# Kernel tuning notes

Measured on AMD Instinct MI355X. Metric: run time of the kernel, lower is better.

## Reference

```python
import jax, jax.numpy as jnp
import numpy as np

N = 50000      # nodes
E = 800000     # edges
G = 512        # graphs
IN = 544; HID = 64; H = 4; OUT = 2
EPS = 1e-5

def setup_inputs():
    key = jax.random.key(0)
    ks = jax.random.split(key, 16)
    x = jax.random.normal(ks[0], (N, IN), jnp.float32)
    edge_index = jax.random.randint(ks[1], (2, E), 0, N, jnp.int64)
    batch = jnp.sort(jax.random.randint(ks[2], (N,), 0, G, jnp.int64))
    s = lambda k, shp, fan: jax.random.normal(k, shp, jnp.float32) / np.sqrt(fan)
    return {
        'x': x, 'edge_index': edge_index, 'batch': batch,
        'ln_g': jnp.ones((32,), jnp.float32), 'ln_b': jnp.zeros((32,), jnp.float32),
        'bn1_g': jnp.ones((512,), jnp.float32), 'bn1_b': jnp.zeros((512,), jnp.float32),
        'Wc': s(ks[3], (16, 512), 512), 'bc': jnp.zeros((16,), jnp.float32),
        'bn2_g': jnp.ones((48,), jnp.float32), 'bn2_b': jnp.zeros((48,), jnp.float32),
        'Wp': s(ks[4], (HID, 48), 48), 'bp': jnp.zeros((HID,), jnp.float32),
        'Wg': s(ks[5], (H * HID, HID), HID),
        'att_src': s(ks[6], (H, HID), HID), 'att_dst': s(ks[7], (H, HID), HID),
        'bg': jnp.zeros((H * HID,), jnp.float32),
        'bn3_g': jnp.ones((H * HID,), jnp.float32), 'bn3_b': jnp.zeros((H * HID,), jnp.float32),
        'W1': s(ks[8], (HID, H * HID), H * HID), 'b1': jnp.zeros((HID,), jnp.float32),
        'W2': s(ks[9], (OUT, HID), HID), 'b2': jnp.zeros((OUT,), jnp.float32),
    }

def _batchnorm(x, g, b):
    mu = jnp.mean(x, axis=0)
    var = jnp.var(x, axis=0)
    return (x - mu) * jax.lax.rsqrt(var + EPS) * g + b

def _forward(x, ln_g, ln_b, bn1_g, bn1_b, Wc, bc, bn2_g, bn2_b, Wp, bp,
             Wg, att_src, att_dst, bg, bn3_g, bn3_b, W1, b1, W2, b2,
             edge_index, batch):
    # feature split + norms
    x_cnn = _batchnorm(x[:, :512], bn1_g, bn1_b)
    f = x[:, 512:]
    mu = jnp.mean(f, axis=-1, keepdims=True)
    var = jnp.var(f, axis=-1, keepdims=True)
    f = (f - mu) * jax.lax.rsqrt(var + EPS) * ln_g + ln_b
    x_cnn = x_cnn @ Wc.T + bc                      # [N,16]
    z = jnp.concatenate([x_cnn, f], axis=1)        # [N,48]
    z = _batchnorm(z, bn2_g, bn2_b)
    z = jax.nn.relu(z @ Wp.T + bp)                 # [N,HID] (dropout=eval identity)
    # GATConv (concat=True, negative_slope=0.2)
    h = (z @ Wg.T).reshape(N, H, HID)              # [N,H,C]
    a_src = jnp.sum(h * att_src, axis=-1)          # [N,H]
    a_dst = jnp.sum(h * att_dst, axis=-1)          # [N,H]
    src, dst = edge_index[0], edge_index[1]
    e = jax.nn.leaky_relu(a_src[src] + a_dst[dst], 0.2)   # [E,H]
    m = jax.ops.segment_max(e, dst, num_segments=N)
    m = jnp.where(jnp.isfinite(m), m, 0.0)
    ex = jnp.exp(e - m[dst])
    s = jax.ops.segment_sum(ex, dst, num_segments=N)
    alpha = ex / jnp.maximum(s, 1e-16)[dst]               # [E,H]
    out = jax.ops.segment_sum(alpha[:, :, None] * h[src], dst, num_segments=N)
    out = out.reshape(N, H * HID) + bg
    # BatchNorm + ELU + mean pool + MLP head
    out = jax.nn.elu(_batchnorm(out, bn3_g, bn3_b))
    cnt = jax.ops.segment_sum(jnp.ones((N,), out.dtype), batch, num_segments=G)
    pooled = jax.ops.segment_sum(out, batch, num_segments=G) / jnp.maximum(cnt, 1.0)[:, None]
    hmlp = jax.nn.relu(pooled @ W1.T + b1)
    return hmlp @ W2.T + b2                        # [G,OUT]

def reference(x, edge_index, batch, ln_g, ln_b, bn1_g, bn1_b, Wc, bc, bn2_g, bn2_b,
              Wp, bp, Wg, att_src, att_dst, bg, bn3_g, bn3_b, W1, b1, W2, b2):
    return _forward(x, ln_g, ln_b, bn1_g, bn1_b, Wc, bc, bn2_g, bn2_b, Wp, bp,
                    Wg, att_src, att_dst, bg, bn3_g, bn3_b, W1, b1, W2, b2,
                    edge_index, batch)
```

## Files before the change

kernel.cpp:

```cpp
#include <hip/hip_runtime.h>

static constexpr int N_   = 50000;
static constexpr int E_   = 800000;
static constexpr int G_   = 512;
static constexpr int IN_  = 544;
static constexpr float EPS_ = 1e-5f;

static constexpr size_t OFF_BN1SUM = 0;
static constexpr size_t OFF_BN1SQ  = 2048;
static constexpr size_t OFF_BN2SUM = 4096;
static constexpr size_t OFF_BN2SQ  = 4288;
static constexpr size_t OFF_BN3SUM = 4480;
static constexpr size_t OFF_BN3SQ  = 5504;
static constexpr size_t OFF_COUNT  = 6528;
static constexpr size_t OFF_CUR    = 206528;
static constexpr size_t ZERO_BYTES = 406528;
static constexpr size_t OFF_OFFS   = 406528;
static constexpr size_t OFF_PART   = 606592;
static constexpr size_t OFF_WC2    = 606848;
static constexpr size_t OFF_C2     = 639616;
static constexpr size_t OFF_WP2    = 639744;
static constexpr size_t OFF_CP     = 652032;
static constexpr size_t OFF_WGT    = 652288;
static constexpr size_t OFF_ASRC   = 719872;
static constexpr size_t OFF_ADST   = 1519872;
static constexpr size_t OFF_SRCS   = 2319872;
static constexpr size_t OFF_Z      = 5519872;
static constexpr size_t OFF_H      = 15119872;
static constexpr size_t OFF_OUTP   = 66319872;
static constexpr size_t OFF_POOL   = 117519872;

#define DEV static __device__ __forceinline__

DEV float lrelu(float v) { return v > 0.f ? v : 0.2f * v; }
DEV unsigned short f2bf(float f) {
    unsigned u = __float_as_uint(f);
    return (unsigned short)((u + 0x7fffu + ((u >> 16) & 1u)) >> 16);
}
DEV float bf2f(unsigned short u) { return __uint_as_float(((unsigned)u) << 16); }

__global__ __launch_bounds__(512) void k_bn1_stats(
        const float* __restrict__ x, float* __restrict__ sum, float* __restrict__ sq) {
    __shared__ float4 ta[512];
    __shared__ float4 tb[512];
    int t = threadIdx.x;
    int cq = t & 127, rsub = t >> 7;
    int c4 = cq << 2;
    float4 a = make_float4(0.f, 0.f, 0.f, 0.f);
    float4 b = make_float4(0.f, 0.f, 0.f, 0.f);
    for (int r = blockIdx.x * 4 + rsub; r < N_; r += gridDim.x * 4) {
        float4 v = *(const float4*)(x + (size_t)r * IN_ + c4);
        a.x += v.x; a.y += v.y; a.z += v.z; a.w += v.w;
        b.x += v.x * v.x; b.y += v.y * v.y; b.z += v.z * v.z; b.w += v.w * v.w;
    }
    ta[t] = a; tb[t] = b;
    __syncthreads();
    if (t < 128) {
        float4 sa = ta[t], sb = tb[t];
#pragma unroll
        for (int r = 1; r < 4; r++) {
            float4 xa = ta[r * 128 + t], xb = tb[r * 128 + t];
            sa.x += xa.x; sa.y += xa.y; sa.z += xa.z; sa.w += xa.w;
            sb.x += xb.x; sb.y += xb.y; sb.z += xb.z; sb.w += xb.w;
        }
        int c = t << 2;
        atomicAdd(&sum[c + 0], sa.x); atomicAdd(&sum[c + 1], sa.y);
        atomicAdd(&sum[c + 2], sa.z); atomicAdd(&sum[c + 3], sa.w);
        atomicAdd(&sq[c + 0], sb.x);  atomicAdd(&sq[c + 1], sb.y);
        atomicAdd(&sq[c + 2], sb.z);  atomicAdd(&sq[c + 3], sb.w);
    }
}

__global__ void k_fold1(const float* __restrict__ sum, const float* __restrict__ sq,
                        const float* __restrict__ g, const float* __restrict__ b,
                        const float* __restrict__ Wc, const float* __restrict__ bc,
                        float* __restrict__ Wc2, float* __restrict__ c2) {
    __shared__ float t1[512];
    int j = threadIdx.x;
    float mu  = sum[j] / (float)N_;
    float var = sq[j] / (float)N_ - mu * mu;
    float s   = g[j] * rsqrtf(var + EPS_);
    t1[j] = b[j] - mu * s;
    for (int i = 0; i < 16; i++) Wc2[j * 16 + i] = Wc[i * 512 + j] * s;
    __syncthreads();
    if (j < 16) {
        float acc = bc[j];
        for (int k = 0; k < 512; k++) acc += t1[k] * Wc[j * 512 + k];
        c2[j] = acc;
    }
}

__global__ __launch_bounds__(512) void k_z(
        const float* __restrict__ x, const float* __restrict__ Wc2g,
        const float* __restrict__ c2g, const float* __restrict__ lng,
        const float* __restrict__ lnb, float* __restrict__ z,
        float* __restrict__ bn2sum, float* __restrict__ bn2sq) {
    __shared__ float wc2[512 * 16];
    __shared__ float c2s[16];
    __shared__ float bsum[48];
    __shared__ float bsq[48];
    int t = threadIdx.x;
    for (int q = t; q < 8192; q += 512) wc2[q] = Wc2g[q];
    if (t < 16) c2s[t] = c2g[t];
    if (t < 48) { bsum[t] = 0.f; bsq[t] = 0.f; }
    __syncthreads();
    int nd = t >> 3, i = t & 7;
    int node = blockIdx.x * 64 + nd;
    bool valid = node < N_;
    int rn = valid ? node : N_ - 1;
    const float4* xr = (const float4*)(x + (size_t)rn * IN_);
    float acc0 = c2s[i], acc1 = c2s[i + 8];
    for (int u = 0; u < 128; u++) {
        float4 xv = xr[u];
        int j4 = u * 4;
        acc0 += xv.x * wc2[(j4 + 0) * 16 + i];
        acc0 += xv.y * wc2[(j4 + 1) * 16 + i];
        acc0 += xv.z * wc2[(j4 + 2) * 16 + i];
        acc0 += xv.w * wc2[(j4 + 3) * 16 + i];
        acc1 += xv.x * wc2[(j4 + 0) * 16 + i + 8];
        acc1 += xv.y * wc2[(j4 + 1) * 16 + i + 8];
        acc1 += xv.z * wc2[(j4 + 2) * 16 + i + 8];
        acc1 += xv.w * wc2[(j4 + 3) * 16 + i + 8];
    }
    float v[4]; float sm = 0.f, sqv = 0.f;
#pragma unroll
    for (int jj = 0; jj < 4; jj++) {
        v[jj] = x[(size_t)rn * IN_ + 512 + i + 8 * jj];
        sm += v[jj]; sqv += v[jj] * v[jj];
    }
    for (int m = 1; m < 8; m <<= 1) {
        sm  += __shfl_xor(sm, m);
        sqv += __shfl_xor(sqv, m);
    }
    float mu  = sm * (1.f / 32.f);
    float var = sqv * (1.f / 32.f) - mu * mu;
    float rs  = rsqrtf(var + EPS_);
    float outc[6];
    outc[0] = acc0; outc[1] = acc1;
#pragma unroll
    for (int jj = 0; jj < 4; jj++) {
        int c = i + 8 * jj;
        outc[2 + jj] = (v[jj] - mu) * rs * lng[c] + lnb[c];
    }
    if (valid) {
        z[node * 48 + i]     = acc0;
        z[node * 48 + i + 8] = acc1;
#pragma unroll
        for (int jj = 0; jj < 4; jj++) z[node * 48 + 16 + i + 8 * jj] = outc[2 + jj];
    }
    float s6[6], q6[6];
#pragma unroll
    for (int k = 0; k < 6; k++) {
        float vv = valid ? outc[k] : 0.f;
        s6[k] = vv; q6[k] = vv * vv;
    }
#pragma unroll
    for (int m = 8; m < 64; m <<= 1) {
#pragma unroll
        for (int k = 0; k < 6; k++) {
            s6[k] += __shfl_xor(s6[k], m);
            q6[k] += __shfl_xor(q6[k], m);
        }
    }
    if ((t & 63) < 8) {
        int cols[6] = { i, i + 8, 16 + i, 24 + i, 32 + i, 40 + i };
#pragma unroll
        for (int k = 0; k < 6; k++) {
            atomicAdd(&bsum[cols[k]], s6[k]);
            atomicAdd(&bsq[cols[k]],  q6[k]);
        }
    }
    __syncthreads();
    if (t < 48) {
        atomicAdd(&bn2sum[t], bsum[t]);
        atomicAdd(&bn2sq[t],  bsq[t]);
    }
}

__global__ void k_fold2(const float* __restrict__ sum, const float* __restrict__ sq,
                        const float* __restrict__ g, const float* __restrict__ b,
                        const float* __restrict__ Wp, const float* __restrict__ bp,
                        float* __restrict__ Wp2, float* __restrict__ cp) {
    __shared__ float t2[48];
    int i = threadIdx.x;
    if (i < 48) {
        float mu  = sum[i] / (float)N_;
        float var = sq[i] / (float)N_ - mu * mu;
        float s   = g[i] * rsqrtf(var + EPS_);
        t2[i] = b[i] - mu * s;
        for (int k = 0; k < 64; k++) Wp2[i * 64 + k] = Wp[k * 48 + i] * s;
    }
    __syncthreads();
    float acc = bp[i];
    for (int j = 0; j < 48; j++) acc += t2[j] * Wp[i * 48 + j];
    cp[i] = acc;
}

__global__ void k_wgt(const float* __restrict__ Wg, float* __restrict__ Wgt) {
    int idx = blockIdx.x * 256 + threadIdx.x;
    if (idx < 16384) {
        int c = idx >> 6, k = idx & 63;
        Wgt[k * 256 + c] = Wg[idx];
    }
}

__global__ __launch_bounds__(512) void k_h2(
        const float* __restrict__ z, const float* __restrict__ Wp2g,
        const float* __restrict__ cpg, const float* __restrict__ Wgtg,
        const float* __restrict__ att_s, const float* __restrict__ att_d,
        ushort4* __restrict__ hbf, float* __restrict__ asrc, float* __restrict__ adst) {
    __shared__ float4 wgh[32 * 64];
    __shared__ float  z1t[128 * 64];
    __shared__ float  wp2[48 * 64];
    __shared__ float  cps[64];
    __shared__ float4 ats[64];
    __shared__ float4 atd[64];
    int t = threadIdx.x;
    int base = blockIdx.x * 128;
    {
        const float4* z4 = (const float4*)(z + (size_t)base * 48);
        float4* zt4 = (float4*)wgh;
        for (int q = t; q < 1536; q += 512) zt4[q] = z4[q];
    }
    for (int q = t; q < 3072; q += 512) wp2[q] = Wp2g[q];
    if (t < 64) {
        cps[t] = cpg[t];
        ats[t] = ((const float4*)att_s)[t];
        atd[t] = ((const float4*)att_d)[t];
    }
    __syncthreads();
    int w = t >> 6, l = t & 63;
    {
        float wpr[48];
#pragma unroll
        for (int j = 0; j < 48; j++) wpr[j] = wp2[j * 64 + l];
        const float* zt = (const float*)wgh;
        for (int p = 0; p < 16; p++) {
            int nd = p * 8 + w;
            float acc = cps[l];
            const float* zr = zt + nd * 48;
#pragma unroll
            for (int j = 0; j < 48; j++) acc += zr[j] * wpr[j];
            z1t[nd * 64 + l] = fmaxf(acc, 0.f);
        }
    }
    const float4* wg4 = (const float4*)Wgtg;
    float4 acc[16];
#pragma unroll
    for (int nd = 0; nd < 16; nd++) acc[nd] = make_float4(0.f, 0.f, 0.f, 0.f);
    for (int half = 0; half < 2; half++) {
        __syncthreads();
        for (int q = t; q < 2048; q += 512) wgh[q] = wg4[half * 2048 + q];
        __syncthreads();
        int kbase = half * 32;
        for (int kk = 0; kk < 32; kk++) {
            float4 wv = wgh[kk * 64 + l];
            int k = kbase + kk;
#pragma unroll
            for (int nd = 0; nd < 16; nd++) {
                float zv = z1t[(w * 16 + nd) * 64 + k];
                acc[nd].x += zv * wv.x; acc[nd].y += zv * wv.y;
                acc[nd].z += zv * wv.z; acc[nd].w += zv * wv.w;
            }
        }
    }
    float4 as4 = ats[l], ad4 = atd[l];
#pragma unroll
    for (int nd = 0; nd < 16; nd++) {
        int node = base + w * 16 + nd;
        if (node < N_) {
            ushort4 hv;
            hv.x = f2bf(acc[nd].x); hv.y = f2bf(acc[nd].y);
            hv.z = f2bf(acc[nd].z); hv.w = f2bf(acc[nd].w);
            hbf[(size_t)node * 64 + l] = hv;
            float pa = acc[nd].x * as4.x + acc[nd].y * as4.y +
                       acc[nd].z * as4.z + acc[nd].w * as4.w;
            float pb = acc[nd].x * ad4.x + acc[nd].y * ad4.y +
                       acc[nd].z * ad4.z + acc[nd].w * ad4.w;
            for (int m = 1; m < 16; m <<= 1) {
                pa += __shfl_xor(pa, m);
                pb += __shfl_xor(pb, m);
            }
            if ((l & 15) == 0) {
                asrc[node * 4 + (l >> 4)] = pa;
                adst[node * 4 + (l >> 4)] = pb;
            }
        }
    }
}

__global__ void k_hist(const int* __restrict__ ei, int* __restrict__ count) {
    int k = blockIdx.x * 256 + threadIdx.x;
    atomicAdd(&count[ei[E_ + k]], 1);
}

__global__ void k_scan1(const int* __restrict__ count, int* __restrict__ offs,
                        int* __restrict__ part) {
    __shared__ int sd[1024];
    int t = threadIdx.x;
    int idx = blockIdx.x * 1024 + t;
    int v = (idx < N_) ? count[idx] : 0;
    sd[t] = v;
    for (int off = 1; off < 1024; off <<= 1) {
        __syncthreads();
        int tmp = (t >= off) ? sd[t - off] : 0;
        __syncthreads();
        sd[t] += tmp;
    }
    if (idx < N_) offs[idx] = sd[t] - v;
    if (t == 1023) part[blockIdx.x] = sd[1023];
}
__global__ void k_scan2(int* __restrict__ part, int nb) {
    if (threadIdx.x == 0) {
        int run = 0;
        for (int i = 0; i < nb; i++) { int tv = part[i]; part[i] = run; run += tv; }
    }
}
__global__ void k_scan3(int* __restrict__ offs, const int* __restrict__ part) {
    int idx = blockIdx.x * 1024 + threadIdx.x;
    if (idx < N_) offs[idx] += part[blockIdx.x];
}

__global__ void k_scatter(const int* __restrict__ ei, const int* __restrict__ offs,
                          int* __restrict__ cur, int* __restrict__ srcsort) {
    int k = blockIdx.x * 256 + threadIdx.x;
    int src = ei[k], dst = ei[E_ + k];
    int pos = offs[dst] + atomicAdd(&cur[dst], 1);
    srcsort[pos] = src;
}

__global__ __launch_bounds__(256) void k_agg(
        const int* __restrict__ count, const int* __restrict__ offs,
        const int* __restrict__ srcsort, const float* __restrict__ asrc,
        const float* __restrict__ adst, const ushort4* __restrict__ hbf,
        const float* __restrict__ bg, float* __restrict__ outpre) {
    int w = threadIdx.x >> 6, l = threadIdx.x & 63;
    int dst = blockIdx.x * 4 + w;
    const float4* asrc4 = (const float4*)asrc;
    float4* out4 = (float4*)outpre;
    float4 bgv = ((const float4*)bg)[l];
    int deg = count[dst];
    if (deg == 0) { out4[dst * 64 + l] = bgv; return; }
    int base = offs[dst];
    float4 ad = ((const float4*)adst)[dst];
    const float NEGINF = -__builtin_inff();
    int my_src = 0;
    float4 my_e = make_float4(NEGINF, NEGINF, NEGINF, NEGINF);
    if (l < deg) {
        my_src = srcsort[base + l];
        float4 a = asrc4[my_src];
        my_e = make_float4(lrelu(a.x + ad.x), lrelu(a.y + ad.y),
                           lrelu(a.z + ad.z), lrelu(a.w + ad.w));
    }
    float4 mx = my_e;
    for (int j = l + 64; j < deg; j += 64) {
        int s2 = srcsort[base + j];
        float4 a = asrc4[s2];
        mx.x = fmaxf(mx.x, lrelu(a.x + ad.x)); mx.y = fmaxf(mx.y, lrelu(a.y + ad.y));
        mx.z = fmaxf(mx.z, lrelu(a.z + ad.z)); mx.w = fmaxf(mx.w, lrelu(a.w + ad.w));
    }
    for (int m = 1; m < 64; m <<= 1) {
        mx.x = fmaxf(mx.x, __shfl_xor(mx.x, m));
        mx.y = fmaxf(mx.y, __shfl_xor(mx.y, m));
        mx.z = fmaxf(mx.z, __shfl_xor(mx.z, m));
        mx.w = fmaxf(mx.w, __shfl_xor(mx.w, m));
    }
    float4 sv = make_float4(0.f, 0.f, 0.f, 0.f);
    if (l < deg) {
        sv.x = __expf(my_e.x - mx.x); sv.y = __expf(my_e.y - mx.y);
        sv.z = __expf(my_e.z - mx.z); sv.w = __expf(my_e.w - mx.w);
    }
    for (int j = l + 64; j < deg; j += 64) {
        int s2 = srcsort[base + j];
        float4 a = asrc4[s2];
        sv.x += __expf(lrelu(a.x + ad.x) - mx.x);
        sv.y += __expf(lrelu(a.y + ad.y) - mx.y);
        sv.z += __expf(lrelu(a.z + ad.z) - mx.z);
        sv.w += __expf(lrelu(a.w + ad.w) - mx.w);
    }
    for (int m = 1; m < 64; m <<= 1) {
        sv.x += __shfl_xor(sv.x, m); sv.y += __shfl_xor(sv.y, m);
        sv.z += __shfl_xor(sv.z, m); sv.w += __shfl_xor(sv.w, m);
    }
    int hd = l >> 4;
    float mh  = hd == 0 ? mx.x : hd == 1 ? mx.y : hd == 2 ? mx.z : mx.w;
    float sh  = hd == 0 ? sv.x : hd == 1 ? sv.y : hd == 2 ? sv.z : sv.w;
    float adh = hd == 0 ? ad.x : hd == 1 ? ad.y : hd == 2 ? ad.z : ad.w;
    float inv = 1.f / fmaxf(sh, 1e-16f);
    float4 acc = make_float4(0.f, 0.f, 0.f, 0.f);
    for (int j = 0; j < deg; j++) {
        int src; float eh;
        if (j < 64) {
            src = __shfl(my_src, j);
            float ex_ = __shfl(my_e.x, j), ey_ = __shfl(my_e.y, j);
            float ez_ = __shfl(my_e.z, j), ew_ = __shfl(my_e.w, j);
            eh = hd == 0 ? ex_ : hd == 1 ? ey_ : hd == 2 ? ez_ : ew_;
        } else {
            src = srcsort[base + j];
            float4 a = asrc4[src];
            float ah = hd == 0 ? a.x : hd == 1 ? a.y : hd == 2 ? a.z : a.w;
            eh = lrelu(ah + adh);
        }
        float wgt = __expf(eh - mh) * inv;
        ushort4 hv = hbf[(size_t)src * 64 + l];
        acc.x += wgt * bf2f(hv.x); acc.y += wgt * bf2f(hv.y);
        acc.z += wgt * bf2f(hv.z); acc.w += wgt * bf2f(hv.w);
    }
    out4[dst * 64 + l] = make_float4(acc.x + bgv.x, acc.y + bgv.y,
                                     acc.z + bgv.z, acc.w + bgv.w);
}

__global__ __launch_bounds__(256) void k_bn3_stats(
        const float* __restrict__ op, float* __restrict__ sum, float* __restrict__ sq) {
    __shared__ float4 ta[256];
    __shared__ float4 tb[256];
    int t = threadIdx.x;
    int cq = t & 63, rsub = t >> 6;
    int c4 = cq << 2;
    float4 a = make_float4(0.f, 0.f, 0.f, 0.f);
    float4 b = make_float4(0.f, 0.f, 0.f, 0.f);
    for (int r = blockIdx.x * 4 + rsub; r < N_; r += gridDim.x * 4) {
        float4 v = *(const float4*)(op + (size_t)r * 256 + c4);
        a.x += v.x; a.y += v.y; a.z += v.z; a.w += v.w;
        b.x += v.x * v.x; b.y += v.y * v.y; b.z += v.z * v.z; b.w += v.w * v.w;
    }
    ta[t] = a; tb[t] = b;
    __syncthreads();
    if (t < 64) {
        float4 sa = ta[t], sb = tb[t];
#pragma unroll
        for (int r = 1; r < 4; r++) {
            float4 xa = ta[r * 64 + t], xb = tb[r * 64 + t];
            sa.x += xa.x; sa.y += xa.y; sa.z += xa.z; sa.w += xa.w;
            sb.x += xb.x; sb.y += xb.y; sb.z += xb.z; sb.w += xb.w;
        }
        int c = t << 2;
        atomicAdd(&sum[c + 0], sa.x); atomicAdd(&sum[c + 1], sa.y);
        atomicAdd(&sum[c + 2], sa.z); atomicAdd(&sum[c + 3], sa.w);
        atomicAdd(&sq[c + 0], sb.x);  atomicAdd(&sq[c + 1], sb.y);
        atomicAdd(&sq[c + 2], sb.z);  atomicAdd(&sq[c + 3], sb.w);
    }
}

__global__ __launch_bounds__(256) void k_pool(
        const float* __restrict__ op, const int* __restrict__ batch,
        const float* __restrict__ bn3sum, const float* __restrict__ bn3sq,
        const float* __restrict__ bn3g, const float* __restrict__ bn3b,
        float* __restrict__ pooled) {
    __shared__ float4 tile[256];
    int g = blockIdx.x;
    int t = threadIdx.x;
    int cq = t & 63, rsub = t >> 6;
    int c4 = cq << 2;
    int lo = 0, hi = N_;
    while (lo < hi) { int mid = (lo + hi) >> 1; if (batch[mid] < g) lo = mid + 1; else hi = mid; }
    int start = lo;
    hi = N_;
    while (lo < hi) { int mid = (lo + hi) >> 1; if (batch[mid] < g + 1) lo = mid + 1; else hi = mid; }
    int end = lo;
    float scv[4], shv[4];
#pragma unroll
    for (int k = 0; k < 4; k++) {
        int c = c4 + k;
        float mu  = bn3sum[c] / (float)N_;
        float var = bn3sq[c] / (float)N_ - mu * mu;
        float s   = bn3g[c] * rsqrtf(var + EPS_);
        scv[k] = s; shv[k] = bn3b[c] - mu * s;
    }
    float4 acc = make_float4(0.f, 0.f, 0.f, 0.f);
    for (int n = start + rsub; n < end; n += 4) {
        float4 v = *(const float4*)(op + (size_t)n * 256 + c4);
        float e0 = v.x * scv[0] + shv[0], e1 = v.y * scv[1] + shv[1];
        float e2 = v.z * scv[2] + shv[2], e3 = v.w * scv[3] + shv[3];
        acc.x += (e0 > 0.f) ? e0 : expm1f(e0);
        acc.y += (e1 > 0.f) ? e1 : expm1f(e1);
        acc.z += (e2 > 0.f) ? e2 : expm1f(e2);
        acc.w += (e3 > 0.f) ? e3 : expm1f(e3);
    }
    tile[t] = acc;
    __syncthreads();
    if (t < 64) {
        float4 s = tile[t];
#pragma unroll
        for (int r = 1; r < 4; r++) {
            float4 xv = tile[r * 64 + t];
            s.x += xv.x; s.y += xv.y; s.z += xv.z; s.w += xv.w;
        }
        float cn = fmaxf((float)(end - start), 1.f);
        float icn = 1.f / cn;
        ((float4*)(pooled + (size_t)g * 256))[t] =
            make_float4(s.x * icn, s.y * icn, s.z * icn, s.w * icn);
    }
}

__global__ void k_mlp(const float* __restrict__ pooled, const float* __restrict__ W1,
                      const float* __restrict__ b1, const float* __restrict__ W2,
                      const float* __restrict__ b2, float* __restrict__ out) {
    __shared__ float pl[256];
    __shared__ float hm[64];
    int g = blockIdx.x;
    int i = threadIdx.x;
    for (int q = i; q < 256; q += 64) pl[q] = pooled[g * 256 + q];
    __syncthreads();
    float acc = b1[i];
    for (int c = 0; c < 256; c++) acc += pl[c] * W1[i * 256 + c];
    hm[i] = fmaxf(acc, 0.f);
    __syncthreads();
    if (i < 2) {
        float a = b2[i];
        for (int k = 0; k < 64; k++) a += hm[k] * W2[i * 64 + k];
        out[g * 2 + i] = a;
    }
}

extern "C" void kernel_launch(void* const* d_in, const int* in_sizes, int n_in,
                              void* d_out, int out_size, void* d_ws, size_t ws_size,
                              hipStream_t stream) {
    const float* x    = (const float*)d_in[0];
    const int*   ei   = (const int*)d_in[1];
    const int*   batch= (const int*)d_in[2];
    const float* lng  = (const float*)d_in[3];
    const float* lnb  = (const float*)d_in[4];
    const float* bn1g = (const float*)d_in[5];
    const float* bn1b = (const float*)d_in[6];
    const float* Wc   = (const float*)d_in[7];
    const float* bc   = (const float*)d_in[8];
    const float* bn2g = (const float*)d_in[9];
    const float* bn2b = (const float*)d_in[10];
    const float* Wp   = (const float*)d_in[11];
    const float* bp   = (const float*)d_in[12];
    const float* Wg   = (const float*)d_in[13];
    const float* atts = (const float*)d_in[14];
    const float* attd = (const float*)d_in[15];
    const float* bg   = (const float*)d_in[16];
    const float* bn3g = (const float*)d_in[17];
    const float* bn3b = (const float*)d_in[18];
    const float* W1   = (const float*)d_in[19];
    const float* b1   = (const float*)d_in[20];
    const float* W2   = (const float*)d_in[21];
    const float* b2   = (const float*)d_in[22];
    float* out = (float*)d_out;

    char* w8 = (char*)d_ws;
    float* bn1sum = (float*)(w8 + OFF_BN1SUM);
    float* bn1sq  = (float*)(w8 + OFF_BN1SQ);
    float* bn2sum = (float*)(w8 + OFF_BN2SUM);
    float* bn2sq  = (float*)(w8 + OFF_BN2SQ);
    float* bn3sum = (float*)(w8 + OFF_BN3SUM);
    float* bn3sq  = (float*)(w8 + OFF_BN3SQ);
    int*   count  = (int*)(w8 + OFF_COUNT);
    int*   cur    = (int*)(w8 + OFF_CUR);
    int*   offs   = (int*)(w8 + OFF_OFFS);
    int*   part   = (int*)(w8 + OFF_PART);
    float* Wc2    = (float*)(w8 + OFF_WC2);
    float* c2     = (float*)(w8 + OFF_C2);
    float* Wp2    = (float*)(w8 + OFF_WP2);
    float* cp     = (float*)(w8 + OFF_CP);
    float* Wgt    = (float*)(w8 + OFF_WGT);
    float* asrc   = (float*)(w8 + OFF_ASRC);
    float* adst   = (float*)(w8 + OFF_ADST);
    int*   srcs   = (int*)(w8 + OFF_SRCS);
    float* z      = (float*)(w8 + OFF_Z);
    ushort4* hbf  = (ushort4*)(w8 + OFF_H);
    float* outp   = (float*)(w8 + OFF_OUTP);
    float* pooled = (float*)(w8 + OFF_POOL);

    hipMemsetAsync(d_ws, 0, ZERO_BYTES, stream);

    k_bn1_stats<<<256, 512, 0, stream>>>(x, bn1sum, bn1sq);
    k_fold1<<<1, 512, 0, stream>>>(bn1sum, bn1sq, bn1g, bn1b, Wc, bc, Wc2, c2);
    k_z<<<(N_ + 63) / 64, 512, 0, stream>>>(x, Wc2, c2, lng, lnb, z, bn2sum, bn2sq);
    k_fold2<<<1, 64, 0, stream>>>(bn2sum, bn2sq, bn2g, bn2b, Wp, bp, Wp2, cp);
    k_wgt<<<64, 256, 0, stream>>>(Wg, Wgt);
    k_h2<<<(N_ + 127) / 128, 512, 0, stream>>>(z, Wp2, cp, Wgt, atts, attd, hbf, asrc, adst);
    k_hist<<<E_ / 256, 256, 0, stream>>>(ei, count);
    const int SCANB = (N_ + 1023) / 1024;
    k_scan1<<<SCANB, 1024, 0, stream>>>(count, offs, part);
    k_scan2<<<1, 64, 0, stream>>>(part, SCANB);
    k_scan3<<<SCANB, 1024, 0, stream>>>(offs, part);
    k_scatter<<<E_ / 256, 256, 0, stream>>>(ei, offs, cur, srcs);
    k_agg<<<N_ / 4, 256, 0, stream>>>(count, offs, srcs, asrc, adst, hbf, bg, outp);
    k_bn3_stats<<<256, 256, 0, stream>>>(outp, bn3sum, bn3sq);
    k_pool<<<G_, 256, 0, stream>>>(outp, batch, bn3sum, bn3sq, bn3g, bn3b, pooled);
    k_mlp<<<G_, 64, 0, stream>>>(pooled, W1, b1, W2, b2, out);
}
```

Before: 582.6 us.

## Fuse small kernels, transpose Wc2 for vector LDS reads, cache softmax weights in agg

Several small launches are merged: the edge histogram runs in extra blocks of the BN1-stats kernel, scan2/scan3 become one kernel, fold2 absorbs the Wg transpose, and pooling absorbs the MLP head. k_z now stores the folded Wc2 transposed with a padded stride so each thread reads float4 weights. k_agg keeps the first 128 sources and their exp weights in shared memory, so the aggregation loop skips the shuffles and exp recomputation. The goal is lower launch overhead and less redundant per-edge work, at the cost of more shared memory per block and more complex kernels.

```diff
diff --git a/kernel.cpp b/kernel.cpp
--- a/kernel.cpp
+++ b/kernel.cpp
@@ -37,18 +37,24 @@
     unsigned u = __float_as_uint(f);
     return (unsigned short)((u + 0x7fffu + ((u >> 16) & 1u)) >> 16);
 }
-DEV float bf2f(unsigned short u) { return __uint_as_float(((unsigned)u) << 16); }
-
-__global__ __launch_bounds__(512) void k_bn1_stats(
-        const float* __restrict__ x, float* __restrict__ sum, float* __restrict__ sq) {
+
+__global__ __launch_bounds__(512) void k_bn1_hist(
+        const float* __restrict__ x, float* __restrict__ sum, float* __restrict__ sq,
+        const int* __restrict__ ei, int* __restrict__ count) {
     __shared__ float4 ta[512];
     __shared__ float4 tb[512];
+    int bid = blockIdx.x;
     int t = threadIdx.x;
+    if (bid >= 256) {
+        int k = (bid - 256) * 512 + t;
+        if (k < E_) atomicAdd(&count[ei[E_ + k]], 1);
+        return;
+    }
     int cq = t & 127, rsub = t >> 7;
     int c4 = cq << 2;
     float4 a = make_float4(0.f, 0.f, 0.f, 0.f);
     float4 b = make_float4(0.f, 0.f, 0.f, 0.f);
-    for (int r = blockIdx.x * 4 + rsub; r < N_; r += gridDim.x * 4) {
+    for (int r = bid * 4 + rsub; r < N_; r += 256 * 4) {
         float4 v = *(const float4*)(x + (size_t)r * IN_ + c4);
         a.x += v.x; a.y += v.y; a.z += v.z; a.w += v.w;
         b.x += v.x * v.x; b.y += v.y * v.y; b.z += v.z * v.z; b.w += v.w * v.w;
@@ -71,36 +77,45 @@
     }
 }
 
-__global__ void k_fold1(const float* __restrict__ sum, const float* __restrict__ sq,
-                        const float* __restrict__ g, const float* __restrict__ b,
-                        const float* __restrict__ Wc, const float* __restrict__ bc,
-                        float* __restrict__ Wc2, float* __restrict__ c2) {
-    __shared__ float t1[512];
+__global__ __launch_bounds__(512) void k_fold1(
+        const float* __restrict__ sum, const float* __restrict__ sq,
+        const float* __restrict__ g, const float* __restrict__ b,
+        const float* __restrict__ Wc, const float* __restrict__ bc,
+        float* __restrict__ Wc2t, float* __restrict__ c2) {
+    __shared__ float c2s[16];
     int j = threadIdx.x;
+    if (j < 16) c2s[j] = 0.f;
     float mu  = sum[j] / (float)N_;
     float var = sq[j] / (float)N_ - mu * mu;
     float s   = g[j] * rsqrtf(var + EPS_);
-    t1[j] = b[j] - mu * s;
-    for (int i = 0; i < 16; i++) Wc2[j * 16 + i] = Wc[i * 512 + j] * s;
-    __syncthreads();
-    if (j < 16) {
-        float acc = bc[j];
-        for (int k = 0; k < 512; k++) acc += t1[k] * Wc[j * 512 + k];
-        c2[j] = acc;
-    }
-}
-
+    float tj  = b[j] - mu * s;
+    __syncthreads();
+    for (int i = 0; i < 16; i++) {
+        float wv = Wc[i * 512 + j];
+        Wc2t[i * 512 + j] = wv * s;
+        float p = tj * wv;
+        for (int m = 1; m < 64; m <<= 1) p += __shfl_xor(p, m);
+        if ((j & 63) == 0) atomicAdd(&c2s[i], p);
+    }
+    __syncthreads();
+    if (j < 16) c2[j] = c2s[j] + bc[j];
+}
+
+static constexpr int WSTRIDE = 516;
 __global__ __launch_bounds__(512) void k_z(
-        const float* __restrict__ x, const float* __restrict__ Wc2g,
+        const float* __restrict__ x, const float* __restrict__ Wc2tg,
         const float* __restrict__ c2g, const float* __restrict__ lng,
         const float* __restrict__ lnb, float* __restrict__ z,
         float* __restrict__ bn2sum, float* __restrict__ bn2sq) {
-    __shared__ float wc2[512 * 16];
+    __shared__ float wc2[16 * WSTRIDE];
     __shared__ float c2s[16];
     __shared__ float bsum[48];
     __shared__ float bsq[48];
     int t = threadIdx.x;
-    for (int q = t; q < 8192; q += 512) wc2[q] = Wc2g[q];
+    for (int q = t; q < 8192; q += 512) {
+        int row = q >> 9, col = q & 511;
+        wc2[row * WSTRIDE + col] = Wc2tg[q];
+    }
     if (t < 16) c2s[t] = c2g[t];
     if (t < 48) { bsum[t] = 0.f; bsq[t] = 0.f; }
     __syncthreads();
@@ -109,18 +124,15 @@
     bool valid = node < N_;
     int rn = valid ? node : N_ - 1;
     const float4* xr = (const float4*)(x + (size_t)rn * IN_);
+    const float4* w0 = (const float4*)(wc2 + i * WSTRIDE);
+    const float4* w1 = (const float4*)(wc2 + (i + 8) * WSTRIDE);
     float acc0 = c2s[i], acc1 = c2s[i + 8];
     for (int u = 0; u < 128; u++) {
         float4 xv = xr[u];
-        int j4 = u * 4;
-        acc0 += xv.x * wc2[(j4 + 0) * 16 + i];
-        acc0 += xv.y * wc2[(j4 + 1) * 16 + i];
-        acc0 += xv.z * wc2[(j4 + 2) * 16 + i];
-        acc0 += xv.w * wc2[(j4 + 3) * 16 + i];
-        acc1 += xv.x * wc2[(j4 + 0) * 16 + i + 8];
-        acc1 += xv.y * wc2[(j4 + 1) * 16 + i + 8];
-        acc1 += xv.z * wc2[(j4 + 2) * 16 + i + 8];
-        acc1 += xv.w * wc2[(j4 + 3) * 16 + i + 8];
+        float4 a4 = w0[u];
+        float4 b4 = w1[u];
+        acc0 += xv.x * a4.x + xv.y * a4.y + xv.z * a4.z + xv.w * a4.w;
+        acc1 += xv.x * b4.x + xv.y * b4.y + xv.z * b4.z + xv.w * b4.w;
     }
     float v[4]; float sm = 0.f, sqv = 0.f;
 #pragma unroll
@@ -177,31 +189,70 @@
     }
 }
 
-__global__ void k_fold2(const float* __restrict__ sum, const float* __restrict__ sq,
-                        const float* __restrict__ g, const float* __restrict__ b,
-                        const float* __restrict__ Wp, const float* __restrict__ bp,
-                        float* __restrict__ Wp2, float* __restrict__ cp) {
+__global__ __launch_bounds__(256) void k_fold2_wgt(
+        const float* __restrict__ sum, const float* __restrict__ sq,
+        const float* __restrict__ g, const float* __restrict__ b,
+        const float* __restrict__ Wp, const float* __restrict__ bp,
+        float* __restrict__ Wp2, float* __restrict__ cp,
+        const float* __restrict__ Wg, float* __restrict__ Wgt) {
     __shared__ float t2[48];
-    int i = threadIdx.x;
-    if (i < 48) {
-        float mu  = sum[i] / (float)N_;
-        float var = sq[i] / (float)N_ - mu * mu;
-        float s   = g[i] * rsqrtf(var + EPS_);
-        t2[i] = b[i] - mu * s;
-        for (int k = 0; k < 64; k++) Wp2[i * 64 + k] = Wp[k * 48 + i] * s;
-    }
-    __syncthreads();
-    float acc = bp[i];
-    for (int j = 0; j < 48; j++) acc += t2[j] * Wp[i * 48 + j];
-    cp[i] = acc;
-}
-
-__global__ void k_wgt(const float* __restrict__ Wg, float* __restrict__ Wgt) {
-    int idx = blockIdx.x * 256 + threadIdx.x;
-    if (idx < 16384) {
+    int t = threadIdx.x;
+    if (blockIdx.x > 0) {
+        int idx = (blockIdx.x - 1) * 256 + t;
         int c = idx >> 6, k = idx & 63;
         Wgt[k * 256 + c] = Wg[idx];
-    }
+        return;
+    }
+    if (t < 48) {
+        float mu  = sum[t] / (float)N_;
+        float var = sq[t] / (float)N_ - mu * mu;
+        float s   = g[t] * rsqrtf(var + EPS_);
+        t2[t] = b[t] - mu * s;
+        for (int k = 0; k < 64; k++) Wp2[t * 64 + k] = Wp[k * 48 + t] * s;
+    }
+    __syncthreads();
+    if (t < 64) {
+        float acc = bp[t];
+        for (int j = 0; j < 48; j++) acc += t2[j] * Wp[t * 48 + j];
+        cp[t] = acc;
+    }
+}
+
+__global__ void k_scan1(const int* __restrict__ count, int* __restrict__ offs,
+                        int* __restrict__ part) {
+    __shared__ int sd[1024];
+    int t = threadIdx.x;
+    int idx = blockIdx.x * 1024 + t;
+    int v = (idx < N_) ? count[idx] : 0;
+    sd[t] = v;
+    for (int off = 1; off < 1024; off <<= 1) {
+        __syncthreads();
+        int tmp = (t >= off) ? sd[t - off] : 0;
+        __syncthreads();
+        sd[t] += tmp;
+    }
+    if (idx < N_) offs[idx] = sd[t] - v;
+    if (t == 1023) part[blockIdx.x] = sd[1023];
+}
+__global__ void k_scan23(int* __restrict__ offs, const int* __restrict__ part) {
+    __shared__ int bs;
+    int t = threadIdx.x, b = blockIdx.x;
+    if (t < 64) {
+        int v = (t < b) ? part[t] : 0;
+        for (int m = 1; m < 64; m <<= 1) v += __shfl_xor(v, m);
+        if (t == 0) bs = v;
+    }
+    __syncthreads();
+    int idx = b * 1024 + t;
+    if (idx < N_) offs[idx] += bs;
+}
+
+__global__ void k_scatter(const int* __restrict__ ei, const int* __restrict__ offs,
+                          int* __restrict__ cur, int* __restrict__ srcsort) {
+    int k = blockIdx.x * 256 + threadIdx.x;
+    int src = ei[k], dst = ei[E_ + k];
+    int pos = offs[dst] + atomicAdd(&cur[dst], 1);
+    srcsort[pos] = src;
 }
 
 __global__ __launch_bounds__(512) void k_h2(
@@ -289,51 +340,13 @@
     }
 }
 
-__global__ void k_hist(const int* __restrict__ ei, int* __restrict__ count) {
-    int k = blockIdx.x * 256 + threadIdx.x;
-    atomicAdd(&count[ei[E_ + k]], 1);
-}
-
-__global__ void k_scan1(const int* __restrict__ count, int* __restrict__ offs,
-                        int* __restrict__ part) {
-    __shared__ int sd[1024];
-    int t = threadIdx.x;
-    int idx = blockIdx.x * 1024 + t;
-    int v = (idx < N_) ? count[idx] : 0;
-    sd[t] = v;
-    for (int off = 1; off < 1024; off <<= 1) {
-        __syncthreads();
-        int tmp = (t >= off) ? sd[t - off] : 0;
-        __syncthreads();
-        sd[t] += tmp;
-    }
-    if (idx < N_) offs[idx] = sd[t] - v;
-    if (t == 1023) part[blockIdx.x] = sd[1023];
-}
-__global__ void k_scan2(int* __restrict__ part, int nb) {
-    if (threadIdx.x == 0) {
-        int run = 0;
-        for (int i = 0; i < nb; i++) { int tv = part[i]; part[i] = run; run += tv; }
-    }
-}
-__global__ void k_scan3(int* __restrict__ offs, const int* __restrict__ part) {
-    int idx = blockIdx.x * 1024 + threadIdx.x;
-    if (idx < N_) offs[idx] += part[blockIdx.x];
-}
-
-__global__ void k_scatter(const int* __restrict__ ei, const int* __restrict__ offs,
-                          int* __restrict__ cur, int* __restrict__ srcsort) {
-    int k = blockIdx.x * 256 + threadIdx.x;
-    int src = ei[k], dst = ei[E_ + k];
-    int pos = offs[dst] + atomicAdd(&cur[dst], 1);
-    srcsort[pos] = src;
-}
-
 __global__ __launch_bounds__(256) void k_agg(
         const int* __restrict__ count, const int* __restrict__ offs,
         const int* __restrict__ srcsort, const float* __restrict__ asrc,
         const float* __restrict__ adst, const ushort4* __restrict__ hbf,
         const float* __restrict__ bg, float* __restrict__ outpre) {
+    __shared__ int   s_src[4][128];
+    __shared__ float s_wf[4][512];
     int w = threadIdx.x >> 6, l = threadIdx.x & 63;
     int dst = blockIdx.x * 4 + w;
     const float4* asrc4 = (const float4*)asrc;
@@ -344,16 +357,25 @@
     int base = offs[dst];
     float4 ad = ((const float4*)adst)[dst];
     const float NEGINF = -__builtin_inff();
-    int my_src = 0;
-    float4 my_e = make_float4(NEGINF, NEGINF, NEGINF, NEGINF);
+    float4 e0 = make_float4(NEGINF, NEGINF, NEGINF, NEGINF);
+    float4 e1 = make_float4(NEGINF, NEGINF, NEGINF, NEGINF);
     if (l < deg) {
-        my_src = srcsort[base + l];
-        float4 a = asrc4[my_src];
-        my_e = make_float4(lrelu(a.x + ad.x), lrelu(a.y + ad.y),
-                           lrelu(a.z + ad.z), lrelu(a.w + ad.w));
-    }
-    float4 mx = my_e;
-    for (int j = l + 64; j < deg; j += 64) {
+        int s0 = srcsort[base + l];
+        s_src[w][l] = s0;
+        float4 a = asrc4[s0];
+        e0 = make_float4(lrelu(a.x + ad.x), lrelu(a.y + ad.y),
+                         lrelu(a.z + ad.z), lrelu(a.w + ad.w));
+    }
+    if (l + 64 < deg) {
+        int s1 = srcsort[base + l + 64];
+        s_src[w][l + 64] = s1;
+        float4 a = asrc4[s1];
+        e1 = make_float4(lrelu(a.x + ad.x), lrelu(a.y + ad.y),
+                         lrelu(a.z + ad.z), lrelu(a.w + ad.w));
+    }
+    float4 mx = make_float4(fmaxf(e0.x, e1.x), fmaxf(e0.y, e1.y),
+                            fmaxf(e0.z, e1.z), fmaxf(e0.w, e1.w));
+    for (int j = l + 128; j < deg; j += 64) {
         int s2 = srcsort[base + j];
         float4 a = asrc4[s2];
         mx.x = fmaxf(mx.x, lrelu(a.x + ad.x)); mx.y = fmaxf(mx.y, lrelu(a.y + ad.y));
@@ -367,10 +389,18 @@
     }
     float4 sv = make_float4(0.f, 0.f, 0.f, 0.f);
     if (l < deg) {
-        sv.x = __expf(my_e.x - mx.x); sv.y = __expf(my_e.y - mx.y);
-        sv.z = __expf(my_e.z - mx.z); sv.w = __expf(my_e.w - mx.w);
-    }
-    for (int j = l + 64; j < deg; j += 64) {
+        float4 ex = make_float4(__expf(e0.x - mx.x), __expf(e0.y - mx.y),
+                                __expf(e0.z - mx.z), __expf(e0.w - mx.w));
+        *(float4*)&s_wf[w][l * 4] = ex;
+        sv.x += ex.x; sv.y += ex.y; sv.z += ex.z; sv.w += ex.w;
+    }
+    if (l + 64 < deg) {
+        float4 ex = make_float4(__expf(e1.x - mx.x), __expf(e1.y - mx.y),
+                                __expf(e1.z - mx.z), __expf(e1.w - mx.w));
+        *(float4*)&s_wf[w][(l + 64) * 4] = ex;
+        sv.x += ex.x; sv.y += ex.y; sv.z += ex.z; sv.w += ex.w;
+    }
+    for (int j = l + 128; j < deg; j += 64) {
         int s2 = srcsort[base + j];
         float4 a = asrc4[s2];
         sv.x += __expf(lrelu(a.x + ad.x) - mx.x);
@@ -387,27 +417,32 @@
     float sh  = hd == 0 ? sv.x : hd == 1 ? sv.y : hd == 2 ? sv.z : sv.w;
     float adh = hd == 0 ? ad.x : hd == 1 ? ad.y : hd == 2 ? ad.z : ad.w;
     float inv = 1.f / fmaxf(sh, 1e-16f);
-    float4 acc = make_float4(0.f, 0.f, 0.f, 0.f);
-    for (int j = 0; j < deg; j++) {
-        int src; float eh;
-        if (j < 64) {
-            src = __shfl(my_src, j);
-            float ex_ = __shfl(my_e.x, j), ey_ = __shfl(my_e.y, j);
-            float ez_ = __shfl(my_e.z, j), ew_ = __shfl(my_e.w, j);
-            eh = hd == 0 ? ex_ : hd == 1 ? ey_ : hd == 2 ? ez_ : ew_;
-        } else {
-            src = srcsort[base + j];
-            float4 a = asrc4[src];
-            float ah = hd == 0 ? a.x : hd == 1 ? a.y : hd == 2 ? a.z : a.w;
-            eh = lrelu(ah + adh);
-        }
-        float wgt = __expf(eh - mh) * inv;
-        ushort4 hv = hbf[(size_t)src * 64 + l];
-        acc.x += wgt * bf2f(hv.x); acc.y += wgt * bf2f(hv.y);
-        acc.z += wgt * bf2f(hv.z); acc.w += wgt * bf2f(hv.w);
-    }
-    out4[dst * 64 + l] = make_float4(acc.x + bgv.x, acc.y + bgv.y,
-                                     acc.z + bgv.z, acc.w + bgv.w);
+    float4 accv = make_float4(0.f, 0.f, 0.f, 0.f);
+    const uint2* h2p = (const uint2*)hbf;
+    int dcap = deg < 128 ? deg : 128;
+#pragma unroll 2
+    for (int j = 0; j < dcap; j++) {
+        int src = s_src[w][j];
+        float wgt = s_wf[w][j * 4 + hd] * inv;
+        uint2 u = h2p[(size_t)src * 64 + l];
+        accv.x += wgt * __uint_as_float(u.x << 16);
+        accv.y += wgt * __uint_as_float(u.x & 0xffff0000u);
+        accv.z += wgt * __uint_as_float(u.y << 16);
+        accv.w += wgt * __uint_as_float(u.y & 0xffff0000u);
+    }
+    for (int j = 128; j < deg; j++) {
+        int src = srcsort[base + j];
+        float4 a = asrc4[src];
+        float ah = hd == 0 ? a.x : hd == 1 ? a.y : hd == 2 ? a.z : a.w;
+        float wgt = __expf(lrelu(ah + adh) - mh) * inv;
+        uint2 u = h2p[(size_t)src * 64 + l];
+        accv.x += wgt * __uint_as_float(u.x << 16);
+        accv.y += wgt * __uint_as_float(u.x & 0xffff0000u);
+        accv.z += wgt * __uint_as_float(u.y << 16);
+        accv.w += wgt * __uint_as_float(u.y & 0xffff0000u);
+    }
+    out4[dst * 64 + l] = make_float4(accv.x + bgv.x, accv.y + bgv.y,
+                                     accv.z + bgv.z, accv.w + bgv.w);
 }
 
 __global__ __launch_bounds__(256) void k_bn3_stats(
@@ -442,12 +477,16 @@
     }
 }
 
-__global__ __launch_bounds__(256) void k_pool(
+__global__ __launch_bounds__(256) void k_pool_mlp(
         const float* __restrict__ op, const int* __restrict__ batch,
         const float* __restrict__ bn3sum, const float* __restrict__ bn3sq,
         const float* __restrict__ bn3g, const float* __restrict__ bn3b,
-        float* __restrict__ pooled) {
+        const float* __restrict__ W1, const float* __restrict__ b1,
+        const float* __restrict__ W2, const float* __restrict__ b2,
+        float* __restrict__ out) {
     __shared__ float4 tile[256];
+    __shared__ float  pl[256];
+    __shared__ float  hm[64];
     int g = blockIdx.x;
     int t = threadIdx.x;
     int cq = t & 63, rsub = t >> 6;
@@ -486,30 +525,27 @@
             float4 xv = tile[r * 64 + t];
             s.x += xv.x; s.y += xv.y; s.z += xv.z; s.w += xv.w;
         }
-        float cn = fmaxf((float)(end - start), 1.f);
-        float icn = 1.f / cn;
-        ((float4*)(pooled + (size_t)g * 256))[t] =
-            make_float4(s.x * icn, s.y * icn, s.z * icn, s.w * icn);
-    }
-}
-
-__global__ void k_mlp(const float* __restrict__ pooled, const float* __restrict__ W1,
-                      const float* __restrict__ b1, const float* __restrict__ W2,
-                      const float* __restrict__ b2, float* __restrict__ out) {
-    __shared__ float pl[256];
-    __shared__ float hm[64];
-    int g = blockIdx.x;
-    int i = threadIdx.x;
-    for (int q = i; q < 256; q += 64) pl[q] = pooled[g * 256 + q];
-    __syncthreads();
-    float acc = b1[i];
-    for (int c = 0; c < 256; c++) acc += pl[c] * W1[i * 256 + c];
-    hm[i] = fmaxf(acc, 0.f);
-    __syncthreads();
-    if (i < 2) {
-        float a = b2[i];
-        for (int k = 0; k < 64; k++) a += hm[k] * W2[i * 64 + k];
-        out[g * 2 + i] = a;
+        float icn = 1.f / fmaxf((float)(end - start), 1.f);
+        ((float4*)pl)[t] = make_float4(s.x * icn, s.y * icn, s.z * icn, s.w * icn);
+    }
+    __syncthreads();
+    {
+        int j = t >> 2, part = t & 3;
+        const float* w1r = W1 + j * 256 + part * 64;
+        const float* plr = pl + part * 64;
+        float a = 0.f;
+#pragma unroll
+        for (int c = 0; c < 64; c++) a += w1r[c] * plr[c];
+        a += __shfl_xor(a, 1);
+        a += __shfl_xor(a, 2);
+        if (part == 0) hm[j] = fmaxf(a + b1[j], 0.f);
+    }
+    __syncthreads();
+    if (t < 128) {
+        int j = t >> 6, k = t & 63;
+        float p = W2[j * 64 + k] * hm[k];
+        for (int m = 1; m < 64; m <<= 1) p += __shfl_xor(p, m);
+        if (k == 0) out[g * 2 + j] = p + b2[j];
     }
 }
 
@@ -552,7 +588,7 @@
     int*   cur    = (int*)(w8 + OFF_CUR);
     int*   offs   = (int*)(w8 + OFF_OFFS);
     int*   part   = (int*)(w8 + OFF_PART);
-    float* Wc2    = (float*)(w8 + OFF_WC2);
+    float* Wc2t   = (float*)(w8 + OFF_WC2);
     float* c2     = (float*)(w8 + OFF_C2);
     float* Wp2    = (float*)(w8 + OFF_WP2);
     float* cp     = (float*)(w8 + OFF_CP);
@@ -563,24 +599,21 @@
     float* z      = (float*)(w8 + OFF_Z);
     ushort4* hbf  = (ushort4*)(w8 + OFF_H);
     float* outp   = (float*)(w8 + OFF_OUTP);
-    float* pooled = (float*)(w8 + OFF_POOL);
 
     hipMemsetAsync(d_ws, 0, ZERO_BYTES, stream);
 
-    k_bn1_stats<<<256, 512, 0, stream>>>(x, bn1sum, bn1sq);
-    k_fold1<<<1, 512, 0, stream>>>(bn1sum, bn1sq, bn1g, bn1b, Wc, bc, Wc2, c2);
-    k_z<<<(N_ + 63) / 64, 512, 0, stream>>>(x, Wc2, c2, lng, lnb, z, bn2sum, bn2sq);
-    k_fold2<<<1, 64, 0, stream>>>(bn2sum, bn2sq, bn2g, bn2b, Wp, bp, Wp2, cp);
-    k_wgt<<<64, 256, 0, stream>>>(Wg, Wgt);
-    k_h2<<<(N_ + 127) / 128, 512, 0, stream>>>(z, Wp2, cp, Wgt, atts, attd, hbf, asrc, adst);
-    k_hist<<<E_ / 256, 256, 0, stream>>>(ei, count);
+    const int HISTB = (E_ + 511) / 512;
+    k_bn1_hist<<<256 + HISTB, 512, 0, stream>>>(x, bn1sum, bn1sq, ei, count);
+    k_fold1<<<1, 512, 0, stream>>>(bn1sum, bn1sq, bn1g, bn1b, Wc, bc, Wc2t, c2);
+    k_z<<<(N_ + 63) / 64, 512, 0, stream>>>(x, Wc2t, c2, lng, lnb, z, bn2sum, bn2sq);
     const int SCANB = (N_ + 1023) / 1024;
     k_scan1<<<SCANB, 1024, 0, stream>>>(count, offs, part);
-    k_scan2<<<1, 64, 0, stream>>>(part, SCANB);
-    k_scan3<<<SCANB, 1024, 0, stream>>>(offs, part);
+    k_scan23<<<SCANB, 1024, 0, stream>>>(offs, part);
+    k_fold2_wgt<<<65, 256, 0, stream>>>(bn2sum, bn2sq, bn2g, bn2b, Wp, bp, Wp2, cp, Wg, Wgt);
     k_scatter<<<E_ / 256, 256, 0, stream>>>(ei, offs, cur, srcs);
+    k_h2<<<(N_ + 127) / 128, 512, 0, stream>>>(z, Wp2, cp, Wgt, atts, attd, hbf, asrc, adst);
     k_agg<<<N_ / 4, 256, 0, stream>>>(count, offs, srcs, asrc, adst, hbf, bg, outp);
     k_bn3_stats<<<256, 256, 0, stream>>>(outp, bn3sum, bn3sq);
-    k_pool<<<G_, 256, 0, stream>>>(outp, batch, bn3sum, bn3sq, bn3g, bn3b, pooled);
-    k_mlp<<<G_, 64, 0, stream>>>(pooled, W1, b1, W2, b2, out);
-}
+    k_pool_mlp<<<G_, 256, 0, stream>>>(outp, batch, bn3sum, bn3sq, bn3g, bn3b,
+                                       W1, b1, W2, b2, out);
+}
```

Result: faster. 555.0 us (-4.8%).
